# Kernel optimization log

Hardware: AMD Instinct MI355X
Metric: run time of the kernel (lower is better)

Reference implementation:

```python
import jax, jax.numpy as jnp
import numpy as np

B, L, K, I, O = 4, 10000, 16, 256, 256


def setup_inputs() -> dict:
    key = jax.random.key(0)
    k1, k2, k3 = jax.random.split(key, 3)
    x = jax.random.normal(k1, (B, L, I), dtype=jnp.float32)
    index_tensor = jax.random.randint(k2, (L, K), 0, L, dtype=jnp.int64)
    stdv = 0.5
    mask = jax.random.uniform(k3, (K, I, O), dtype=jnp.float32, minval=-stdv, maxval=stdv)
    bias = jnp.zeros((O,), dtype=jnp.float32)
    return {"x": x, "index_tensor": index_tensor, "mask": mask, "bias": bias}


def reference(x, index_tensor, mask, bias):
    # torch: expand x to [b,l,l,i], gather along dim2 with index[l,k] -> [b,l,k,i]
    # equivalent: per output node n, neighbors x[:, index_tensor[n, j], :]
    gathered = x[:, index_tensor, :]            # [b, l, k, i]
    # flatten(k,i) @ flatten(mask: [k*i, o]) == einsum over k,i
    y = jnp.einsum('blki,kio->blo', gathered, mask) + bias
    return y
```

## Files before the change

kernel.cpp:

```cpp
#include <hip/hip_runtime.h>

#define Bdim 4
#define Ldim 10000
#define Kdim 16
#define Idim 256
#define Odim 256

typedef __attribute__((ext_vector_type(8))) __bf16 bf16x8;
typedef __attribute__((ext_vector_type(4))) float f32x4;

__global__ __launch_bounds__(256)
void prepack(const float* __restrict__ x, const float* __restrict__ mask,
             __bf16* __restrict__ xb, __bf16* __restrict__ wpk)
{
    const int b = blockIdx.x;
    if (b < 2500) {
        const size_t base = ((size_t)b * 256 + threadIdx.x) * 16;
#pragma unroll
        for (int j = 0; j < 2; ++j) {
            const float4 f0 = *(const float4*)(x + base + j * 8);
            const float4 f1 = *(const float4*)(x + base + j * 8 + 4);
            bf16x8 v;
            v[0] = (__bf16)f0.x; v[1] = (__bf16)f0.y; v[2] = (__bf16)f0.z; v[3] = (__bf16)f0.w;
            v[4] = (__bf16)f1.x; v[5] = (__bf16)f1.y; v[6] = (__bf16)f1.z; v[7] = (__bf16)f1.w;
            *(bf16x8*)(xb + base + j * 8) = v;
        }
    } else {
        const int tg = (b - 2500) * 256 + threadIdx.x;
        const int c  = tg >> 6;
        const int ln = tg & 63;
        const int ni  = c & 3;
        const int ks  = (c >> 2) & 1;
        const int wid = (c >> 3) & 3;
        const int kb  = c >> 5;
        const int n   = wid * 64 + ni * 16 + (ln & 15);
        const int kk0 = kb * 64 + ks * 32 + (ln >> 4) * 8;
        bf16x8 v;
#pragma unroll
        for (int j = 0; j < 8; ++j)
            v[j] = (__bf16)mask[(size_t)(kk0 + j) * Odim + n];
        *(bf16x8*)(wpk + (size_t)tg * 8) = v;
    }
}

#define TL 16
#define BM 64
#define LDA 72

__global__ __launch_bounds__(256, 3)
void piconv_gemm(const __bf16* __restrict__ xb,
                 const int* __restrict__ idxT,
                 const __bf16* __restrict__ wpk,
                 const float* __restrict__ bias,
                 float* __restrict__ out)
{
    __shared__ __bf16 Alds[2][BM * LDA];
    __shared__ int    idx_lds[TL * Kdim];

    const int t    = threadIdx.x;
    const int l0   = blockIdx.x * TL;
    const int lane = t & 63;
    const int wid  = t >> 6;
    const int q    = lane >> 4;
    const int r16  = lane & 15;

    idx_lds[t] = idxT[l0 * Kdim + t];

    const int arow  = t >> 2;
    const int apart = t & 3;
    const int alt   = arow & 15;
    const int abb   = arow >> 4;
    const size_t abase = ((size_t)abb * Ldim) << 8;

    const __bf16* wbase = wpk + ((size_t)(wid * 8) << 9) + lane * 8;

    f32x4  acc[4][4] = {};
    bf16x8 aN0, aN1, wA[8], wB[8];

    __syncthreads();

    {
        const int iv = idx_lds[alt * Kdim];
        const __bf16* s = xb + abase + (((size_t)iv) << 8) + apart * 16;
        aN0 = *(const bf16x8*)s;
        aN1 = *(const bf16x8*)(s + 8);
#pragma unroll
        for (int j = 0; j < 8; ++j)
            wA[j] = *(const bf16x8*)(wbase + j * 512);
    }

#define STEP(KB, BUF, WCUR, WNXT, PF)                                           \
    {                                                                           \
        *(bf16x8*)&Alds[BUF][arow * LDA + apart * 16]     = aN0;                \
        *(bf16x8*)&Alds[BUF][arow * LDA + apart * 16 + 8] = aN1;                \
        __syncthreads();                                                        \
        if (PF) {                                                               \
            const int kn = ((KB) + 1) >> 2;                                     \
            const int io = ((((KB) + 1) & 3) << 6) + apart * 16;                \
            const int iv = idx_lds[alt * Kdim + kn];                            \
            const __bf16* s = xb + abase + (((size_t)iv) << 8) + io;            \
            aN0 = *(const bf16x8*)s;                                            \
            aN1 = *(const bf16x8*)(s + 8);                                      \
            const __bf16* wq = wbase + ((size_t)((KB) + 1)) * 16384;            \
            _Pragma("unroll")                                                   \
            for (int j = 0; j < 8; ++j)                                         \
                WNXT[j] = *(const bf16x8*)(wq + j * 512);                       \
        }                                                                       \
        _Pragma("unroll")                                                       \
        for (int ks = 0; ks < 2; ++ks) {                                        \
            bf16x8 af[4];                                                       \
            _Pragma("unroll")                                                   \
            for (int mi = 0; mi < 4; ++mi)                                      \
                af[mi] = *(bf16x8*)&Alds[BUF][(mi * 16 + r16) * LDA + ks * 32 + q * 8]; \
            _Pragma("unroll")                                                   \
            for (int mi = 0; mi < 4; ++mi)                                      \
                _Pragma("unroll")                                               \
                for (int ni = 0; ni < 4; ++ni)                                  \
                    acc[mi][ni] = __builtin_amdgcn_mfma_f32_16x16x32_bf16(      \
                        af[mi], WCUR[ks * 4 + ni], acc[mi][ni], 0, 0, 0);       \
        }                                                                       \
    }

    for (int kb2 = 0; kb2 < 32; ++kb2) {
        STEP(2 * kb2,     0, wA, wB, true)
        STEP(2 * kb2 + 1, 1, wB, wA, (2 * kb2 + 1) < 63)
    }
#undef STEP

    float bv[4];
#pragma unroll
    for (int ni = 0; ni < 4; ++ni)
        bv[ni] = bias[wid * 64 + ni * 16 + r16];
#pragma unroll
    for (int mi = 0; mi < 4; ++mi) {
#pragma unroll
        for (int rr = 0; rr < 4; ++rr) {
            const int lt = q * 4 + rr;
            float* dst = out + (((size_t)(mi * Ldim + l0 + lt)) << 8) + wid * 64 + r16;
#pragma unroll
            for (int ni = 0; ni < 4; ++ni)
                dst[ni * 16] = acc[mi][ni][rr] + bv[ni];
        }
    }
}

#define FTL 32
#define FBN 128
#define FLDA 72
__global__ __launch_bounds__(256)
void piconv_fallback(const float* __restrict__ x,
                     const int* __restrict__ idxT,
                     const float* __restrict__ mask,
                     const float* __restrict__ bias,
                     float* __restrict__ out)
{
    __shared__ __bf16 Alds[128 * FLDA];
    __shared__ __bf16 Wlds[FBN * FLDA];
    const int t  = threadIdx.x;
    const int l0 = blockIdx.x * FTL;
    const int n0 = blockIdx.y * FBN;
    const int lane = t & 63;
    const int wid  = t >> 6;
    const int wm   = wid >> 1;
    const int wn   = wid & 1;
    const int q    = lane >> 4;
    const int r16  = lane & 15;
    f32x4 acc[4][4] = {};
    const int am    = t >> 1;
    const int ahalf = t & 1;
    const int alt   = am & 31;
    const int abb   = am >> 5;
    const int al    = l0 + alt;
    const bool avalid = (al < Ldim);
    for (int kb = 0; kb < 64; ++kb) {
        {
            const int ksl = kb >> 2;
            const int i0  = ((kb & 3) << 6) + (ahalf << 5);
            const int idx = avalid ? idxT[al * Kdim + ksl] : 0;
            const float* src = x + (((size_t)(abb * Ldim + idx)) << 8) + i0;
#pragma unroll
            for (int j = 0; j < 4; ++j) {
                const float4 f0 = *(const float4*)(src + j * 8);
                const float4 f1 = *(const float4*)(src + j * 8 + 4);
                bf16x8 v;
                v[0] = (__bf16)f0.x; v[1] = (__bf16)f0.y; v[2] = (__bf16)f0.z; v[3] = (__bf16)f0.w;
                v[4] = (__bf16)f1.x; v[5] = (__bf16)f1.y; v[6] = (__bf16)f1.z; v[7] = (__bf16)f1.w;
                *(bf16x8*)&Alds[am * FLDA + (ahalf << 5) + j * 8] = v;
            }
        }
        {
#pragma unroll
            for (int it = 0; it < 4; ++it) {
                const int pair = t + it * 256;
                const int n    = pair & 127;
                const int g    = pair >> 7;
                const float* src = mask + (((size_t)(kb * 64 + g * 8)) << 8) + n0 + n;
                bf16x8 v;
#pragma unroll
                for (int j = 0; j < 8; ++j)
                    v[j] = (__bf16)src[(size_t)j << 8];
                *(bf16x8*)&Wlds[n * FLDA + g * 8] = v;
            }
        }
        __syncthreads();
#pragma unroll
        for (int ks = 0; ks < 2; ++ks) {
            bf16x8 af[4], bfr[4];
#pragma unroll
            for (int mi = 0; mi < 4; ++mi)
                af[mi] = *(bf16x8*)&Alds[(wm * 64 + mi * 16 + r16) * FLDA + ks * 32 + q * 8];
#pragma unroll
            for (int ni = 0; ni < 4; ++ni)
                bfr[ni] = *(bf16x8*)&Wlds[(wn * 64 + ni * 16 + r16) * FLDA + ks * 32 + q * 8];
#pragma unroll
            for (int mi = 0; mi < 4; ++mi)
#pragma unroll
                for (int ni = 0; ni < 4; ++ni)
                    acc[mi][ni] = __builtin_amdgcn_mfma_f32_16x16x32_bf16(
                        af[mi], bfr[ni], acc[mi][ni], 0, 0, 0);
        }
        __syncthreads();
    }
    float bv[4];
#pragma unroll
    for (int ni = 0; ni < 4; ++ni)
        bv[ni] = bias[n0 + wn * 64 + ni * 16 + r16];
#pragma unroll
    for (int mi = 0; mi < 4; ++mi) {
        const int mrow = wm * 64 + mi * 16 + q * 4;
#pragma unroll
        for (int rr = 0; rr < 4; ++rr) {
            const int m  = mrow + rr;
            const int lt = m & 31;
            const int bb = m >> 5;
            const int l  = l0 + lt;
            if (l < Ldim) {
                float* dst = out + (((size_t)(bb * Ldim + l)) << 8) + n0 + wn * 64 + r16;
#pragma unroll
                for (int ni = 0; ni < 4; ++ni)
                    dst[ni * 16] = acc[mi][ni][rr] + bv[ni];
            }
        }
    }
}

extern "C" void kernel_launch(void* const* d_in, const int* in_sizes, int n_in,
                              void* d_out, int out_size, void* d_ws, size_t ws_size,
                              hipStream_t stream) {
    const float* x    = (const float*)d_in[0];
    const int*   idx  = (const int*)d_in[1];
    const float* mask = (const float*)d_in[2];
    const float* bias = (const float*)d_in[3];
    float* out = (float*)d_out;

    const size_t xb_bytes = (size_t)Bdim * Ldim * Idim * 2;
    const size_t wp_bytes = (size_t)Kdim * Idim * Odim * 2;

    if (ws_size >= xb_bytes + wp_bytes) {
        __bf16* xb  = (__bf16*)d_ws;
        __bf16* wpk = (__bf16*)((char*)d_ws + xb_bytes);
        prepack<<<2500 + 512, 256, 0, stream>>>(x, mask, xb, wpk);
        piconv_gemm<<<Ldim / TL, 256, 0, stream>>>(xb, idx, wpk, bias, out);
    } else {
        dim3 grid((Ldim + FTL - 1) / FTL, Odim / FBN, 1);
        piconv_fallback<<<grid, 256, 0, stream>>>(x, idx, mask, bias, out);
    }
}
```

Baseline: 191.6 us.

## Deepen A-tile pipeline to four LDS buffers with half the barriers

Moves the gathered-A staging from a double buffer to a four-stage LDS ring. Global gathers are issued two steps ahead in two register sets, and the block synchronises only every other k-step using a raw s_barrier after an lgkmcnt wait. The aim is to hide gather latency better and cut barrier stalls in the MFMA main loop. It doubles A-tile LDS use, which may lower occupancy, and it relies on the hand-written barrier and stage indexing being correct for the write-after-read hazards.

```diff
diff --git a/kernel.cpp b/kernel.cpp
--- a/kernel.cpp
+++ b/kernel.cpp
@@ -47,6 +47,9 @@
 #define BM 64
 #define LDA 72
 
+#define BARRIER() do { asm volatile("s_waitcnt lgkmcnt(0)" ::: "memory"); \
+                       __builtin_amdgcn_s_barrier(); } while (0)
+
 __global__ __launch_bounds__(256, 3)
 void piconv_gemm(const __bf16* __restrict__ xb,
                  const int* __restrict__ idxT,
@@ -54,7 +57,7 @@
                  const float* __restrict__ bias,
                  float* __restrict__ out)
 {
-    __shared__ __bf16 Alds[2][BM * LDA];
+    __shared__ __bf16 Alds[4][BM * LDA];
     __shared__ int    idx_lds[TL * Kdim];
 
     const int t    = threadIdx.x;
@@ -75,43 +78,60 @@
     const __bf16* wbase = wpk + ((size_t)(wid * 8) << 9) + lane * 8;
 
     f32x4  acc[4][4] = {};
-    bf16x8 aN0, aN1, wA[8], wB[8];
+    bf16x8 aE0, aE1;
+    bf16x8 aO0, aO1;
+    bf16x8 wA[8], wB[8];
 
     __syncthreads();
 
     {
         const int iv = idx_lds[alt * Kdim];
         const __bf16* s = xb + abase + (((size_t)iv) << 8) + apart * 16;
-        aN0 = *(const bf16x8*)s;
-        aN1 = *(const bf16x8*)(s + 8);
+        const bf16x8 t0 = *(const bf16x8*)(s);
+        const bf16x8 t1 = *(const bf16x8*)(s + 8);
+        const bf16x8 t2 = *(const bf16x8*)(s + 64);
+        const bf16x8 t3 = *(const bf16x8*)(s + 72);
+        *(bf16x8*)&Alds[0][arow * LDA + apart * 16]     = t0;
+        *(bf16x8*)&Alds[0][arow * LDA + apart * 16 + 8] = t1;
+        *(bf16x8*)&Alds[1][arow * LDA + apart * 16]     = t2;
+        *(bf16x8*)&Alds[1][arow * LDA + apart * 16 + 8] = t3;
 #pragma unroll
         for (int j = 0; j < 8; ++j)
             wA[j] = *(const bf16x8*)(wbase + j * 512);
-    }
-
-#define STEP(KB, BUF, WCUR, WNXT, PF)                                           \
+        aE0 = *(const bf16x8*)(s + 128);
+        aE1 = *(const bf16x8*)(s + 136);
+        aO0 = *(const bf16x8*)(s + 192);
+        aO1 = *(const bf16x8*)(s + 200);
+    }
+    __syncthreads();
+
+#define STEP(J, SB, WCUR, WNXT, AR0, AR1, WRF, PAF, PWF)                        \
     {                                                                           \
-        *(bf16x8*)&Alds[BUF][arow * LDA + apart * 16]     = aN0;                \
-        *(bf16x8*)&Alds[BUF][arow * LDA + apart * 16 + 8] = aN1;                \
-        __syncthreads();                                                        \
-        if (PF) {                                                               \
-            const int kn = ((KB) + 1) >> 2;                                     \
-            const int io = ((((KB) + 1) & 3) << 6) + apart * 16;                \
-            const int iv = idx_lds[alt * Kdim + kn];                            \
-            const __bf16* s = xb + abase + (((size_t)iv) << 8) + io;            \
-            aN0 = *(const bf16x8*)s;                                            \
-            aN1 = *(const bf16x8*)(s + 8);                                      \
-            const __bf16* wq = wbase + ((size_t)((KB) + 1)) * 16384;            \
+        if (((J) & 1) == 0) BARRIER();                                          \
+        if (PWF) {                                                              \
+            const __bf16* wq = wbase + ((size_t)((SB) + (J) + 1)) * 16384;      \
             _Pragma("unroll")                                                   \
             for (int j = 0; j < 8; ++j)                                         \
                 WNXT[j] = *(const bf16x8*)(wq + j * 512);                       \
+        }                                                                       \
+        if (WRF) {                                                              \
+            *(bf16x8*)&Alds[((J) + 2) & 3][arow * LDA + apart * 16]     = AR0;  \
+            *(bf16x8*)&Alds[((J) + 2) & 3][arow * LDA + apart * 16 + 8] = AR1;  \
+        }                                                                       \
+        if (PAF) {                                                              \
+            const int T  = (SB) + (J) + 4;                                      \
+            const int iv = idx_lds[alt * Kdim + (T >> 2)];                      \
+            const __bf16* s = xb + abase + (((size_t)iv) << 8)                  \
+                              + (((J) & 3) << 6) + apart * 16;                  \
+            AR0 = *(const bf16x8*)(s);                                          \
+            AR1 = *(const bf16x8*)(s + 8);                                      \
         }                                                                       \
         _Pragma("unroll")                                                       \
         for (int ks = 0; ks < 2; ++ks) {                                        \
             bf16x8 af[4];                                                       \
             _Pragma("unroll")                                                   \
             for (int mi = 0; mi < 4; ++mi)                                      \
-                af[mi] = *(bf16x8*)&Alds[BUF][(mi * 16 + r16) * LDA + ks * 32 + q * 8]; \
+                af[mi] = *(bf16x8*)&Alds[(J) & 3][(mi * 16 + r16) * LDA + ks * 32 + q * 8]; \
             _Pragma("unroll")                                                   \
             for (int mi = 0; mi < 4; ++mi)                                      \
                 _Pragma("unroll")                                               \
@@ -121,10 +141,17 @@
         }                                                                       \
     }
 
-    for (int kb2 = 0; kb2 < 32; ++kb2) {
-        STEP(2 * kb2,     0, wA, wB, true)
-        STEP(2 * kb2 + 1, 1, wB, wA, (2 * kb2 + 1) < 63)
-    }
+    for (int s4 = 0; s4 < 15; ++s4) {
+        const int SB = s4 * 4;
+        STEP(0, SB, wA, wB, aE0, aE1, true, true, true)
+        STEP(1, SB, wB, wA, aO0, aO1, true, true, true)
+        STEP(2, SB, wA, wB, aE0, aE1, true, true, true)
+        STEP(3, SB, wB, wA, aO0, aO1, true, true, true)
+    }
+    STEP(0, 60, wA, wB, aE0, aE1, true,  false, true)
+    STEP(1, 60, wB, wA, aO0, aO1, true,  false, true)
+    STEP(2, 60, wA, wB, aE0, aE1, false, false, true)
+    STEP(3, 60, wB, wA, aO0, aO1, false, false, false)
 #undef STEP
 
     float bv[4];
```

After: 185.2 us. 3.3% less time.
